# Optimization experiments

Measured on AMD Instinct MI355X. Metric: run time of the kernel, lower is better.

Reference implementation:

```python
import jax, jax.numpy as jnp
import numpy as np

SHIFT = 1
EPS = 1e-5

def setup_inputs() -> dict:
    key = jax.random.key(0)
    k1, k2, k3, k4, k5, k6 = jax.random.split(key, 6)
    B, C, H, Wd = 64, 512, 28, 28
    Cout = 512
    return {
        "x": jax.random.normal(k1, (B, C, H, Wd), dtype=jnp.float32),
        "W": jax.random.normal(k2, (Cout, C), dtype=jnp.float32) * 0.05,
        "gamma": jax.random.uniform(k3, (Cout,), dtype=jnp.float32) + 0.5,
        "beta": jax.random.normal(k4, (Cout,), dtype=jnp.float32) * 0.1,
        "running_mean": jax.random.normal(k5, (Cout,), dtype=jnp.float32) * 0.1,
        "running_var": jax.random.uniform(k6, (Cout,), dtype=jnp.float32) + 0.5,
    }

def reference(x, W, gamma, beta, running_mean, running_var):
    # Group-wise spatial shift: split channels into 4 groups, roll each.
    Cg = x.shape[1] // 4
    x1 = jnp.roll(x[:, 0*Cg:1*Cg], -SHIFT, axis=2)  # up
    x2 = jnp.roll(x[:, 1*Cg:2*Cg],  SHIFT, axis=2)  # down
    x3 = jnp.roll(x[:, 2*Cg:3*Cg], -SHIFT, axis=3)  # left
    x4 = jnp.roll(x[:, 3*Cg:4*Cg],  SHIFT, axis=3)  # right
    shifted = jnp.concatenate([x1, x2, x3, x4], axis=1)  # [B,C,H,W]
    # 1x1 conv (no bias) == channel matmul
    y = jnp.einsum('bchw,oc->bohw', shifted, W)
    # BatchNorm (inference: running stats) folded to scale/shift, then ReLU
    scale = gamma * jax.lax.rsqrt(running_var + EPS)
    shift = beta - running_mean * scale
    y = y * scale[None, :, None, None] + shift[None, :, None, None]
    return jnp.maximum(y, 0.0)
```

## Files before the change

### kernel.cpp

```cpp
#include <hip/hip_runtime.h>
#include <hip/hip_bf16.h>

#define BN   64
#define CIN  512
#define COUT 512
#define HW   784
#define NT   128
#define MT   112
#define BK   64
#define TROW 68

typedef __attribute__((ext_vector_type(8))) short short8;
typedef __attribute__((ext_vector_type(4))) float f32x4;

__device__ __forceinline__ unsigned short f2bf(float f) {
    union { float f; unsigned int u; } v; v.f = f;
    unsigned int r = v.u + 0x7fffu + ((v.u >> 16) & 1u);
    return (unsigned short)(r >> 16);
}

__device__ __forceinline__ uint2 pack4(float a, float b, float c, float d) {
    uint2 r;
    r.x = (unsigned int)f2bf(a) | ((unsigned int)f2bf(b) << 16);
    r.y = (unsigned int)f2bf(c) | ((unsigned int)f2bf(d) << 16);
    return r;
}

__device__ __forceinline__ void gl_lds16(const unsigned short* g, unsigned short* l) {
    __builtin_amdgcn_global_load_lds(
        (const __attribute__((address_space(1))) unsigned int*)g,
        (__attribute__((address_space(3))) unsigned int*)l,
        16, 0, 0);
}

__global__ __launch_bounds__(256)
void p1_shift_cvt(const float* __restrict__ x, const float* __restrict__ W,
                  unsigned short* __restrict__ Wb, unsigned short* __restrict__ Xt)
{
    __shared__ unsigned short sT[MT * TROW];
    const int t = threadIdx.x;
    if (blockIdx.z == BN) {
        int wlin = blockIdx.x * 7 + blockIdx.y;
        for (int gi = wlin * 256 + t; gi < (COUT * CIN) / 8; gi += 56 * 256) {
            const float* p = W + (size_t)gi * 8;
            float4 a = *(const float4*)p;
            float4 c = *(const float4*)(p + 4);
            uint2 lo = pack4(a.x, a.y, a.z, a.w);
            uint2 hi = pack4(c.x, c.y, c.z, c.w);
            uint4 v; v.x = lo.x; v.y = lo.y; v.z = hi.x; v.w = hi.y;
            *(uint4*)(Wb + (size_t)gi * 8) = v;
        }
        return;
    }
    const int kk = blockIdx.x;
    const int mt = blockIdx.y;
    const int b  = blockIdx.z;
    const int g  = kk >> 1;
    const int c0 = kk * BK;
    const int hw_base = mt * MT;
    const float* xb = x + (size_t)b * CIN * HW;

    #pragma unroll
    for (int e0 = 0; e0 < 2; ++e0) {
        int e = t + e0 * 256;
        if (e < (BK / 4) * (MT / 4)) {
            int cq = e / 28;
            int mq = e - cq * 28;
            int hw = hw_base + mq * 4;
            const float* src = xb + (size_t)(c0 + cq * 4) * HW;
            float4 v0, v1, v2, v3;
            if (g < 2) {
                int shw = hw + (g == 0 ? 28 : HW - 28);
                if (shw >= HW) shw -= HW;
                v0 = *(const float4*)(src + 0 * HW + shw);
                v1 = *(const float4*)(src + 1 * HW + shw);
                v2 = *(const float4*)(src + 2 * HW + shw);
                v3 = *(const float4*)(src + 3 * HW + shw);
            } else {
                int h  = hw / 28;
                int w0 = hw - h * 28;
                int base = h * 28;
                #pragma unroll
                for (int j = 0; j < 4; ++j) {
                    const float* row = src + j * HW + base;
                    float4 a = *(const float4*)(row + w0);
                    float4 r;
                    if (g == 2) {
                        float ex = row[(w0 + 4 < 28) ? (w0 + 4) : 0];
                        r.x = a.y; r.y = a.z; r.z = a.w; r.w = ex;
                    } else {
                        float ex = row[(w0 == 0) ? 27 : (w0 - 1)];
                        r.x = ex; r.y = a.x; r.z = a.y; r.w = a.z;
                    }
                    if (j == 0) v0 = r; else if (j == 1) v1 = r;
                    else if (j == 2) v2 = r; else v3 = r;
                }
            }
            int m0 = mq * 4;
            *(uint2*)(&sT[(m0 + 0) * TROW + cq * 4]) = pack4(v0.x, v1.x, v2.x, v3.x);
            *(uint2*)(&sT[(m0 + 1) * TROW + cq * 4]) = pack4(v0.y, v1.y, v2.y, v3.y);
            *(uint2*)(&sT[(m0 + 2) * TROW + cq * 4]) = pack4(v0.z, v1.z, v2.z, v3.z);
            *(uint2*)(&sT[(m0 + 3) * TROW + cq * 4]) = pack4(v0.w, v1.w, v2.w, v3.w);
        }
    }
    __syncthreads();

    unsigned short* Xb = Xt + ((size_t)(b * 8 + kk) * HW + hw_base) * BK;
    for (int ch = t; ch < MT * 8; ch += 256) {
        int m = ch >> 3, j = ch & 7;
        uint2 a = *(const uint2*)(&sT[m * TROW + j * 8]);
        uint2 c = *(const uint2*)(&sT[m * TROW + j * 8 + 4]);
        uint4 v; v.x = a.x; v.y = a.y; v.z = c.x; v.w = c.y;
        *(uint4*)(Xb + (size_t)m * BK + j * 8) = v;
    }
}

__global__ __launch_bounds__(256, 2)
void p2_gemm(const unsigned short* __restrict__ Wb, const unsigned short* __restrict__ Xt,
             const float* __restrict__ gamma, const float* __restrict__ beta,
             const float* __restrict__ rmean, const float* __restrict__ rvar,
             float* __restrict__ out)
{
    __shared__ unsigned short sX[2][MT * BK];

    const int t  = threadIdx.x;
    const int id   = blockIdx.x;
    const int ot   = (id >> 3) & 3;
    const int pair = ((id >> 5) << 3) | (id & 7);
    const int mt   = pair % 7;
    const int b    = pair / 7;
    const int o_base  = ot * NT;
    const int hw_base = mt * MT;
    const int lane = t & 63;
    const int wv   = t >> 6;
    const int m16  = lane & 15;
    const int q    = lane >> 4;

    const unsigned short* Xbase = Xt + ((size_t)(b * 8) * HW + hw_base) * BK;

    auto stage = [&](int kk, unsigned short* buf) {
        const unsigned short* Xk = Xbase + (size_t)kk * HW * BK;
        int nci = (wv < 2) ? 4 : 3;
        for (int i = 0; i < nci; ++i) {
            int ci = wv + 4 * i;
            int ch = ci * 64 + lane;
            int hl = ch >> 3, sl = ch & 7;
            int cs = sl ^ (hl & 7);
            gl_lds16(Xk + hl * BK + cs * 8, &buf[ci * 512]);
        }
    };

    stage(0, sX[0]);

    short8 wf[16][2];
    #pragma unroll
    for (int ki = 0; ki < 16; ++ki)
        #pragma unroll
        for (int bo = 0; bo < 2; ++bo) {
            int row = o_base + wv * 32 + bo * 16 + m16;
            wf[ki][bo] = *(const short8*)(Wb + (size_t)row * CIN + ki * 32 + q * 8);
        }

    f32x4 acc[2][7];
    #pragma unroll
    for (int i = 0; i < 2; ++i)
        #pragma unroll
        for (int j = 0; j < 7; ++j)
            acc[i][j] = (f32x4){0.f, 0.f, 0.f, 0.f};

    __syncthreads();

    #pragma unroll
    for (int kk = 0; kk < CIN / BK; ++kk) {
        if (kk < 7) stage(kk + 1, sX[(kk + 1) & 1]);
        const unsigned short* xs = sX[kk & 1];
        #pragma unroll
        for (int ks = 0; ks < 2; ++ks) {
            short8 bf[7];
            #pragma unroll
            for (int bm = 0; bm < 7; ++bm) {
                int m  = bm * 16 + m16;
                int lc = ks * 4 + q;
                int sl = lc ^ (m & 7);
                bf[bm] = *(const short8*)(&xs[m * BK + sl * 8]);
            }
            #pragma unroll
            for (int bm = 0; bm < 7; ++bm) {
                acc[0][bm] = __builtin_amdgcn_mfma_f32_16x16x32_bf16(wf[kk * 2 + ks][0], bf[bm], acc[0][bm], 0, 0, 0);
                acc[1][bm] = __builtin_amdgcn_mfma_f32_16x16x32_bf16(wf[kk * 2 + ks][1], bf[bm], acc[1][bm], 0, 0, 0);
            }
        }
        __syncthreads();
    }

    float scl[2][4], shf[2][4];
    #pragma unroll
    for (int bo = 0; bo < 2; ++bo)
        #pragma unroll
        for (int r = 0; r < 4; ++r) {
            int o = o_base + wv * 32 + bo * 16 + q * 4 + r;
            float sc = gamma[o] * rsqrtf(rvar[o] + 1e-5f);
            scl[bo][r] = sc;
            shf[bo][r] = beta[o] - rmean[o] * sc;
        }
    float* outb = out + (size_t)b * COUT * HW;
    #pragma unroll
    for (int bo = 0; bo < 2; ++bo) {
        #pragma unroll
        for (int r = 0; r < 4; ++r) {
            int o = o_base + wv * 32 + bo * 16 + q * 4 + r;
            float* orow = outb + (size_t)o * HW + hw_base + m16;
            #pragma unroll
            for (int bm = 0; bm < 7; ++bm) {
                float y = acc[bo][bm][r] * scl[bo][r] + shf[bo][r];
                y = fmaxf(y, 0.f);
                __builtin_nontemporal_store(y, orow + bm * 16);
            }
        }
    }
}

#define SW_STRIDE 72
#define SX_STRIDE 64
__global__ __launch_bounds__(256, 2)
void shiftconv_fallback(const float* __restrict__ x, const float* __restrict__ Wf,
                        const float* __restrict__ gamma, const float* __restrict__ beta,
                        const float* __restrict__ rmean, const float* __restrict__ rvar,
                        float* __restrict__ out)
{
    __shared__ unsigned short sW[NT * SW_STRIDE];
    __shared__ unsigned short sX[MT * SX_STRIDE];
    const int t = threadIdx.x;
    const int ot = blockIdx.x, mt = blockIdx.y, b = blockIdx.z;
    const int o_base = ot * NT, hw_base = mt * MT;
    const float* xb = x + (size_t)b * CIN * HW;
    const int lane = t & 63, wv = t >> 6, m16 = lane & 15, q = lane >> 4;
    f32x4 acc[2][7];
    #pragma unroll
    for (int i = 0; i < 2; ++i)
        #pragma unroll
        for (int j = 0; j < 7; ++j) acc[i][j] = (f32x4){0.f, 0.f, 0.f, 0.f};
    #pragma unroll
    for (int kk = 0; kk < CIN / BK; ++kk) {
        const int k0 = kk * BK;
        const int g = k0 >> 7;
        #pragma unroll
        for (int e0 = 0; e0 < 2; ++e0) {
            int e = t + e0 * 256;
            if (e < (BK / 4) * (MT / 4)) {
                int cq = e / 28, mq = e - cq * 28;
                int hw = hw_base + mq * 4;
                const float* src = xb + (size_t)(k0 + cq * 4) * HW;
                float4 v0, v1, v2, v3;
                if (g < 2) {
                    int shw = hw + (g == 0 ? 28 : HW - 28);
                    if (shw >= HW) shw -= HW;
                    v0 = *(const float4*)(src + 0 * HW + shw);
                    v1 = *(const float4*)(src + 1 * HW + shw);
                    v2 = *(const float4*)(src + 2 * HW + shw);
                    v3 = *(const float4*)(src + 3 * HW + shw);
                } else {
                    int h = hw / 28, w0 = hw - h * 28, base = h * 28;
                    #pragma unroll
                    for (int j = 0; j < 4; ++j) {
                        const float* row = src + j * HW + base;
                        float4 a = *(const float4*)(row + w0);
                        float4 r;
                        if (g == 2) {
                            float ex = row[(w0 + 4 < 28) ? (w0 + 4) : 0];
                            r.x = a.y; r.y = a.z; r.z = a.w; r.w = ex;
                        } else {
                            float ex = row[(w0 == 0) ? 27 : (w0 - 1)];
                            r.x = ex; r.y = a.x; r.z = a.y; r.w = a.z;
                        }
                        if (j == 0) v0 = r; else if (j == 1) v1 = r;
                        else if (j == 2) v2 = r; else v3 = r;
                    }
                }
                int m0 = mq * 4;
                { int p = (cq + 5 * (m0 + 0)) & 15;
                  *(uint2*)(&sX[(m0 + 0) * SX_STRIDE + p * 4]) = pack4(v0.x, v1.x, v2.x, v3.x); }
                { int p = (cq + 5 * (m0 + 1)) & 15;
                  *(uint2*)(&sX[(m0 + 1) * SX_STRIDE + p * 4]) = pack4(v0.y, v1.y, v2.y, v3.y); }
                { int p = (cq + 5 * (m0 + 2)) & 15;
                  *(uint2*)(&sX[(m0 + 2) * SX_STRIDE + p * 4]) = pack4(v0.z, v1.z, v2.z, v3.z); }
                { int p = (cq + 5 * (m0 + 3)) & 15;
                  *(uint2*)(&sX[(m0 + 3) * SX_STRIDE + p * 4]) = pack4(v0.w, v1.w, v2.w, v3.w); }
            }
        }
        #pragma unroll
        for (int i = 0; i < 4; ++i) {
            int e = t + i * 256;
            int ol = e >> 3, kg = (e & 7) * 8;
            const float* wr = Wf + (size_t)(o_base + ol) * CIN + k0 + kg;
            float4 a = *(const float4*)(wr);
            float4 c = *(const float4*)(wr + 4);
            uint2 lo = pack4(a.x, a.y, a.z, a.w);
            uint2 hi = pack4(c.x, c.y, c.z, c.w);
            uint4 v; v.x = lo.x; v.y = lo.y; v.z = hi.x; v.w = hi.y;
            *(uint4*)(&sW[ol * SW_STRIDE + kg]) = v;
        }
        __syncthreads();
        #pragma unroll
        for (int ks = 0; ks < BK; ks += 32) {
            short8 afrag[2];
            #pragma unroll
            for (int bo = 0; bo < 2; ++bo) {
                int row = wv * 32 + bo * 16 + m16;
                afrag[bo] = *(const short8*)(&sW[row * SW_STRIDE + ks + q * 8]);
            }
            #pragma unroll
            for (int bm = 0; bm < 7; ++bm) {
                int m = bm * 16 + m16;
                int g0 = (ks >> 2) + 2 * q;
                int p0 = (g0 + 5 * m) & 15;
                int p1 = (g0 + 1 + 5 * m) & 15;
                uint2 lo = *(const uint2*)(&sX[m * SX_STRIDE + p0 * 4]);
                uint2 hi = *(const uint2*)(&sX[m * SX_STRIDE + p1 * 4]);
                union { uint2 u2[2]; short8 s; } fb;
                fb.u2[0] = lo; fb.u2[1] = hi;
                acc[0][bm] = __builtin_amdgcn_mfma_f32_16x16x32_bf16(afrag[0], fb.s, acc[0][bm], 0, 0, 0);
                acc[1][bm] = __builtin_amdgcn_mfma_f32_16x16x32_bf16(afrag[1], fb.s, acc[1][bm], 0, 0, 0);
            }
        }
        __syncthreads();
    }
    float scl[2][4], shf[2][4];
    #pragma unroll
    for (int bo = 0; bo < 2; ++bo)
        #pragma unroll
        for (int r = 0; r < 4; ++r) {
            int o = o_base + wv * 32 + bo * 16 + q * 4 + r;
            float sc = gamma[o] * rsqrtf(rvar[o] + 1e-5f);
            scl[bo][r] = sc;
            shf[bo][r] = beta[o] - rmean[o] * sc;
        }
    float* outb = out + (size_t)b * COUT * HW;
    #pragma unroll
    for (int bo = 0; bo < 2; ++bo)
        #pragma unroll
        for (int r = 0; r < 4; ++r) {
            int o = o_base + wv * 32 + bo * 16 + q * 4 + r;
            float* orow = outb + (size_t)o * HW + hw_base + m16;
            #pragma unroll
            for (int bm = 0; bm < 7; ++bm) {
                float y = acc[bo][bm][r] * scl[bo][r] + shf[bo][r];
                y = fmaxf(y, 0.f);
                __builtin_nontemporal_store(y, orow + bm * 16);
            }
        }
}

extern "C" void kernel_launch(void* const* d_in, const int* in_sizes, int n_in,
                              void* d_out, int out_size, void* d_ws, size_t ws_size,
                              hipStream_t stream)
{
    const float* x     = (const float*)d_in[0];
    const float* W     = (const float*)d_in[1];
    const float* gamma = (const float*)d_in[2];
    const float* beta  = (const float*)d_in[3];
    const float* rmean = (const float*)d_in[4];
    const float* rvar  = (const float*)d_in[5];
    float* out = (float*)d_out;

    const size_t wb_bytes = (size_t)COUT * CIN * 2;
    const size_t xt_bytes = (size_t)BN * CIN * HW * 2;
    if (ws_size >= wb_bytes + xt_bytes) {
        unsigned short* Wb = (unsigned short*)d_ws;
        unsigned short* Xt = (unsigned short*)((char*)d_ws + wb_bytes);
        dim3 g1(8, 7, BN + 1);
        p1_shift_cvt<<<g1, 256, 0, stream>>>(x, W, Wb, Xt);
        p2_gemm<<<1792, 256, 0, stream>>>(Wb, Xt, gamma, beta, rmean, rvar, out);
    } else {
        dim3 grid(COUT / NT, HW / MT, BN);
        shiftconv_fallback<<<grid, 256, 0, stream>>>(x, W, gamma, beta, rmean, rvar, out);
    }
}
```

Baseline: 237.2 us.

## Stream weight fragments per k-step in GEMM and widen shift-convert blocks

The GEMM no longer preloads all 32 weight fragments into registers. It double-buffers two fragment sets per k-step alongside the LDS X staging, using a non-unrolled loop over k pairs, which cuts register pressure and code size. The shift/convert kernel moves to 448 threads so each thread handles exactly one 4x4 tile, and it adds a modulo-17 rotation of the LDS transpose columns to reduce bank conflicts. The trade-off is that weight loads now sit inside the main loop, which adds global-load latency there.

```diff
diff --git a/kernel.cpp b/kernel.cpp
--- a/kernel.cpp
+++ b/kernel.cpp
@@ -33,7 +33,7 @@
         16, 0, 0);
 }
 
-__global__ __launch_bounds__(256)
+__global__ __launch_bounds__(448)
 void p1_shift_cvt(const float* __restrict__ x, const float* __restrict__ W,
                   unsigned short* __restrict__ Wb, unsigned short* __restrict__ Xt)
 {
@@ -41,7 +41,7 @@
     const int t = threadIdx.x;
     if (blockIdx.z == BN) {
         int wlin = blockIdx.x * 7 + blockIdx.y;
-        for (int gi = wlin * 256 + t; gi < (COUT * CIN) / 8; gi += 56 * 256) {
+        for (int gi = wlin * 448 + t; gi < (COUT * CIN) / 8; gi += 56 * 448) {
             const float* p = W + (size_t)gi * 8;
             float4 a = *(const float4*)p;
             float4 c = *(const float4*)(p + 4);
@@ -60,56 +60,58 @@
     const int hw_base = mt * MT;
     const float* xb = x + (size_t)b * CIN * HW;
 
+    {
+        const int cq = t / 28;
+        const int mq = t - cq * 28;
+        const int hw = hw_base + mq * 4;
+        const float* src = xb + (size_t)(c0 + cq * 4) * HW;
+        float4 v0, v1, v2, v3;
+        if (g < 2) {
+            int shw = hw + (g == 0 ? 28 : HW - 28);
+            if (shw >= HW) shw -= HW;
+            v0 = *(const float4*)(src + 0 * HW + shw);
+            v1 = *(const float4*)(src + 1 * HW + shw);
+            v2 = *(const float4*)(src + 2 * HW + shw);
+            v3 = *(const float4*)(src + 3 * HW + shw);
+        } else {
+            int h  = hw / 28;
+            int w0 = hw - h * 28;
+            int base = h * 28;
+            #pragma unroll
+            for (int j = 0; j < 4; ++j) {
+                const float* row = src + j * HW + base;
+                float4 a = *(const float4*)(row + w0);
+                float4 r;
+                if (g == 2) {
+                    float ex = row[(w0 + 4 < 28) ? (w0 + 4) : 0];
+                    r.x = a.y; r.y = a.z; r.z = a.w; r.w = ex;
+                } else {
+                    float ex = row[(w0 == 0) ? 27 : (w0 - 1)];
+                    r.x = ex; r.y = a.x; r.z = a.y; r.w = a.z;
+                }
+                if (j == 0) v0 = r; else if (j == 1) v1 = r;
+                else if (j == 2) v2 = r; else v3 = r;
+            }
+        }
+        const int m0 = mq * 4;
+        const int p  = (cq + mq) % 17;
+        *(uint2*)(&sT[(m0 + 0) * TROW + p * 4]) = pack4(v0.x, v1.x, v2.x, v3.x);
+        *(uint2*)(&sT[(m0 + 1) * TROW + p * 4]) = pack4(v0.y, v1.y, v2.y, v3.y);
+        *(uint2*)(&sT[(m0 + 2) * TROW + p * 4]) = pack4(v0.z, v1.z, v2.z, v3.z);
+        *(uint2*)(&sT[(m0 + 3) * TROW + p * 4]) = pack4(v0.w, v1.w, v2.w, v3.w);
+    }
+    __syncthreads();
+
+    unsigned short* Xb = Xt + ((size_t)(b * 8 + kk) * HW + hw_base) * BK;
     #pragma unroll
     for (int e0 = 0; e0 < 2; ++e0) {
-        int e = t + e0 * 256;
-        if (e < (BK / 4) * (MT / 4)) {
-            int cq = e / 28;
-            int mq = e - cq * 28;
-            int hw = hw_base + mq * 4;
-            const float* src = xb + (size_t)(c0 + cq * 4) * HW;
-            float4 v0, v1, v2, v3;
-            if (g < 2) {
-                int shw = hw + (g == 0 ? 28 : HW - 28);
-                if (shw >= HW) shw -= HW;
-                v0 = *(const float4*)(src + 0 * HW + shw);
-                v1 = *(const float4*)(src + 1 * HW + shw);
-                v2 = *(const float4*)(src + 2 * HW + shw);
-                v3 = *(const float4*)(src + 3 * HW + shw);
-            } else {
-                int h  = hw / 28;
-                int w0 = hw - h * 28;
-                int base = h * 28;
-                #pragma unroll
-                for (int j = 0; j < 4; ++j) {
-                    const float* row = src + j * HW + base;
-                    float4 a = *(const float4*)(row + w0);
-                    float4 r;
-                    if (g == 2) {
-                        float ex = row[(w0 + 4 < 28) ? (w0 + 4) : 0];
-                        r.x = a.y; r.y = a.z; r.z = a.w; r.w = ex;
-                    } else {
-                        float ex = row[(w0 == 0) ? 27 : (w0 - 1)];
-                        r.x = ex; r.y = a.x; r.z = a.y; r.w = a.z;
-                    }
-                    if (j == 0) v0 = r; else if (j == 1) v1 = r;
-                    else if (j == 2) v2 = r; else v3 = r;
-                }
-            }
-            int m0 = mq * 4;
-            *(uint2*)(&sT[(m0 + 0) * TROW + cq * 4]) = pack4(v0.x, v1.x, v2.x, v3.x);
-            *(uint2*)(&sT[(m0 + 1) * TROW + cq * 4]) = pack4(v0.y, v1.y, v2.y, v3.y);
-            *(uint2*)(&sT[(m0 + 2) * TROW + cq * 4]) = pack4(v0.z, v1.z, v2.z, v3.z);
-            *(uint2*)(&sT[(m0 + 3) * TROW + cq * 4]) = pack4(v0.w, v1.w, v2.w, v3.w);
-        }
-    }
-    __syncthreads();
-
-    unsigned short* Xb = Xt + ((size_t)(b * 8 + kk) * HW + hw_base) * BK;
-    for (int ch = t; ch < MT * 8; ch += 256) {
+        int ch = t + e0 * 448;
         int m = ch >> 3, j = ch & 7;
-        uint2 a = *(const uint2*)(&sT[m * TROW + j * 8]);
-        uint2 c = *(const uint2*)(&sT[m * TROW + j * 8 + 4]);
+        int q4 = m >> 2;
+        int p0 = (2 * j + q4) % 17;
+        int p1 = (2 * j + 1 + q4) % 17;
+        uint2 a = *(const uint2*)(&sT[m * TROW + p0 * 4]);
+        uint2 c = *(const uint2*)(&sT[m * TROW + p1 * 4]);
         uint4 v; v.x = a.x; v.y = a.y; v.z = c.x; v.w = c.y;
         *(uint4*)(Xb + (size_t)m * BK + j * 8) = v;
     }
@@ -138,7 +140,8 @@
 
     const unsigned short* Xbase = Xt + ((size_t)(b * 8) * HW + hw_base) * BK;
 
-    auto stage = [&](int kk, unsigned short* buf) {
+    auto stage = [&](int kk, int bufi) {
+        unsigned short* buf = sX[bufi];
         const unsigned short* Xk = Xbase + (size_t)kk * HW * BK;
         int nci = (wv < 2) ? 4 : 3;
         for (int i = 0; i < nci; ++i) {
@@ -150,16 +153,8 @@
         }
     };
 
-    stage(0, sX[0]);
-
-    short8 wf[16][2];
-    #pragma unroll
-    for (int ki = 0; ki < 16; ++ki)
-        #pragma unroll
-        for (int bo = 0; bo < 2; ++bo) {
-            int row = o_base + wv * 32 + bo * 16 + m16;
-            wf[ki][bo] = *(const short8*)(Wb + (size_t)row * CIN + ki * 32 + q * 8);
-        }
+    const unsigned short* wrow0 = Wb + (size_t)(o_base + wv * 32 + m16) * CIN + q * 8;
+    const unsigned short* wrow1 = wrow0 + 16 * CIN;
 
     f32x4 acc[2][7];
     #pragma unroll
@@ -168,30 +163,57 @@
         for (int j = 0; j < 7; ++j)
             acc[i][j] = (f32x4){0.f, 0.f, 0.f, 0.f};
 
+    short8 wc[2][2], wn[2][2];
+    stage(0, 0);
+    wc[0][0] = *(const short8*)(wrow0);
+    wc[0][1] = *(const short8*)(wrow1);
+    wc[1][0] = *(const short8*)(wrow0 + 32);
+    wc[1][1] = *(const short8*)(wrow1 + 32);
     __syncthreads();
 
-    #pragma unroll
-    for (int kk = 0; kk < CIN / BK; ++kk) {
-        if (kk < 7) stage(kk + 1, sX[(kk + 1) & 1]);
-        const unsigned short* xs = sX[kk & 1];
-        #pragma unroll
-        for (int ks = 0; ks < 2; ++ks) {
-            short8 bf[7];
-            #pragma unroll
-            for (int bm = 0; bm < 7; ++bm) {
-                int m  = bm * 16 + m16;
-                int lc = ks * 4 + q;
-                int sl = lc ^ (m & 7);
-                bf[bm] = *(const short8*)(&xs[m * BK + sl * 8]);
-            }
-            #pragma unroll
-            for (int bm = 0; bm < 7; ++bm) {
-                acc[0][bm] = __builtin_amdgcn_mfma_f32_16x16x32_bf16(wf[kk * 2 + ks][0], bf[bm], acc[0][bm], 0, 0, 0);
-                acc[1][bm] = __builtin_amdgcn_mfma_f32_16x16x32_bf16(wf[kk * 2 + ks][1], bf[bm], acc[1][bm], 0, 0, 0);
-            }
-        }
-        __syncthreads();
-    }
+#define COMPUTE(XS, WF)                                                          \
+    {                                                                            \
+        const unsigned short* xs = (XS);                                         \
+        _Pragma("unroll")                                                        \
+        for (int ks = 0; ks < 2; ++ks) {                                         \
+            _Pragma("unroll")                                                    \
+            for (int bm = 0; bm < 7; ++bm) {                                     \
+                int m  = bm * 16 + m16;                                          \
+                int lc = ks * 4 + q;                                             \
+                int sl = lc ^ (m & 7);                                           \
+                short8 bf = *(const short8*)(&xs[m * BK + sl * 8]);              \
+                acc[0][bm] = __builtin_amdgcn_mfma_f32_16x16x32_bf16(WF[ks][0], bf, acc[0][bm], 0, 0, 0); \
+                acc[1][bm] = __builtin_amdgcn_mfma_f32_16x16x32_bf16(WF[ks][1], bf, acc[1][bm], 0, 0, 0); \
+            }                                                                    \
+        }                                                                        \
+    }
+
+    #pragma unroll 1
+    for (int kp = 0; kp < 4; ++kp) {
+        {
+            const int kn = 2 * kp + 1;
+            stage(kn, 1);
+            wn[0][0] = *(const short8*)(wrow0 + kn * 64);
+            wn[0][1] = *(const short8*)(wrow1 + kn * 64);
+            wn[1][0] = *(const short8*)(wrow0 + kn * 64 + 32);
+            wn[1][1] = *(const short8*)(wrow1 + kn * 64 + 32);
+            COMPUTE(sX[0], wc);
+            __syncthreads();
+        }
+        {
+            const int kn = 2 * kp + 2;
+            if (kn < 8) {
+                stage(kn, 0);
+                wc[0][0] = *(const short8*)(wrow0 + kn * 64);
+                wc[0][1] = *(const short8*)(wrow1 + kn * 64);
+                wc[1][0] = *(const short8*)(wrow0 + kn * 64 + 32);
+                wc[1][1] = *(const short8*)(wrow1 + kn * 64 + 32);
+            }
+            COMPUTE(sX[1], wn);
+            __syncthreads();
+        }
+    }
+#undef COMPUTE
 
     float scl[2][4], shf[2][4];
     #pragma unroll
@@ -369,7 +391,7 @@
         unsigned short* Wb = (unsigned short*)d_ws;
         unsigned short* Xt = (unsigned short*)((char*)d_ws + wb_bytes);
         dim3 g1(8, 7, BN + 1);
-        p1_shift_cvt<<<g1, 256, 0, stream>>>(x, W, Wb, Xt);
+        p1_shift_cvt<<<g1, 448, 0, stream>>>(x, W, Wb, Xt);
         p2_gemm<<<1792, 256, 0, stream>>>(Wb, Xt, gamma, beta, rmean, rvar, out);
     } else {
         dim3 grid(COUT / NT, HW / MT, BN);
```

Result: faster. 227.7 us (-4.0%).
